# Kernel tuning notes

Hardware: AMD Instinct MI355X
Metric: run time of the kernel (lower is better)

Reference implementation:

```python
import jax, jax.numpy as jnp
import numpy as np

VOCAB, EMB = 100000, 300
B, T = 64, 128
RNN, OUT = 256, 256

def _structure(seed=0):
    # Deterministic forest: sentence b has length T - b (128..65, sorted descending
    # as required by pack_padded_sequence). Each sentence is a random recursive
    # dependency tree: parent[i] ~ U[0, i). node_level = longest path from a leaf,
    # which equals the dgl.prop_nodes_topo frontier index of the node.
    rng = np.random.default_rng(seed)
    lengths = np.array([T - b for b in range(B)], dtype=np.int64)
    offsets = np.concatenate([[0], np.cumsum(lengths)])
    N = int(offsets[-1])
    level = np.zeros(N, np.int64)
    child, parent, tok = [], [], []
    for b in range(B):
        Lb, base = int(lengths[b]), int(offsets[b])
        par = np.zeros(Lb, np.int64)
        for i in range(1, Lb):
            par[i] = rng.integers(0, i)
        lev = np.zeros(Lb, np.int64)
        for i in range(Lb - 1, 0, -1):  # parent index < child index
            lev[par[i]] = max(lev[par[i]], lev[i] + 1)
        level[base:base + Lb] = lev
        child.append(base + np.arange(1, Lb))
        parent.append(base + par[1:])
        tok.append(b * T + np.arange(Lb))
    return (lengths, np.concatenate(child), np.concatenate(parent),
            np.concatenate(tok), level, int(level.max()) + 1)

def setup_inputs() -> dict:
    key = jax.random.key(0)
    ks = jax.random.split(key, 16)
    lengths, child_idx, parent_idx, tok_idx, node_level, n_levels = _structure()
    s = 0.05
    G4, G3, H2 = 4 * RNN, 3 * OUT, 2 * RNN
    return dict(
        embed_ids=jax.random.randint(ks[0], (B, T), 0, VOCAB),
        lengths=jnp.asarray(lengths),
        child_idx=jnp.asarray(child_idx),
        parent_idx=jnp.asarray(parent_idx),
        tok_idx=jnp.asarray(tok_idx),
        node_level=jnp.asarray(node_level),
        n_levels=n_levels,
        emb_table=jax.random.normal(ks[1], (VOCAB, EMB), jnp.float32) * s,
        w_ih_f=jax.random.normal(ks[2], (G4, EMB), jnp.float32) * s,
        w_hh_f=jax.random.normal(ks[3], (G4, RNN), jnp.float32) * s,
        b_f=jax.random.normal(ks[4], (G4,), jnp.float32) * s,
        w_ih_b=jax.random.normal(ks[5], (G4, EMB), jnp.float32) * s,
        w_hh_b=jax.random.normal(ks[6], (G4, RNN), jnp.float32) * s,
        b_b=jax.random.normal(ks[7], (G4,), jnp.float32) * s,
        W_iou=jax.random.normal(ks[8], (G3, H2), jnp.float32) * s,
        U_iou=jax.random.normal(ks[9], (G3, OUT), jnp.float32) * s,
        b_iou=jax.random.normal(ks[10], (G3,), jnp.float32) * s,
        U_f=jax.random.normal(ks[11], (OUT, OUT), jnp.float32) * s,
        b_uf=jax.random.normal(ks[12], (OUT,), jnp.float32) * s,
        W_hid=jax.random.normal(ks[13], (OUT, H2), jnp.float32) * s,
        b_hid=jax.random.normal(ks[14], (OUT,), jnp.float32) * s,
    )

def _lstm(x, Wih, Whh, b):
    # x: [B, T, E] -> hidden states [B, T, H]; PyTorch gate order i, f, g, o
    Bn, H = x.shape[0], Whh.shape[1]
    def step(carry, xt):
        h, c = carry
        g = xt @ Wih.T + h @ Whh.T + b
        i, f, gg, o = jnp.split(g, 4, axis=-1)
        c = jax.nn.sigmoid(f) * c + jax.nn.sigmoid(i) * jnp.tanh(gg)
        h = jax.nn.sigmoid(o) * jnp.tanh(c)
        return (h, c), h
    h0 = jnp.zeros((Bn, H), x.dtype)
    _, hs = jax.lax.scan(step, (h0, h0), jnp.swapaxes(x, 0, 1))
    return jnp.swapaxes(hs, 0, 1)

def _forward(embed_ids, lengths, child_idx, parent_idx, tok_idx, node_level, n_levels,
             emb_table, w_ih_f, w_hh_f, b_f, w_ih_b, w_hh_b, b_b,
             W_iou, U_iou, b_iou, U_f, b_uf, W_hid, b_hid):
    x = emb_table[embed_ids]                                  # [B,T,E]; dropout = identity (eval)
    h_f = _lstm(x, w_ih_f, w_hh_f, b_f)
    # Backward direction over TRUE lengths only (pack_padded semantics):
    # per-row involution t -> len-1-t for t < len, identity on padding.
    t = jnp.arange(T)
    ridx = jnp.where(t[None, :] < lengths[:, None], lengths[:, None] - 1 - t[None, :], t[None, :])
    x_rev = jnp.take_along_axis(x, ridx[:, :, None], axis=1)
    h_b = jnp.take_along_axis(_lstm(x_rev, w_ih_b, w_hh_b, b_b), ridx[:, :, None], axis=1)
    h_seq = jnp.concatenate([h_f, h_b], axis=-1).reshape(B * T, 2 * RNN)
    hx = h_seq[tok_idx]                                       # [N, 2*RNN] valid tokens, flattened
    N = hx.shape[0]
    iou_acc = hx @ W_iou.T                                    # g.ndata['iou'] (W_iou has no bias)
    h = hx @ W_hid.T + b_hid                                  # initial g.ndata['h'] (overwritten by apply)
    c = jnp.zeros((N, OUT), hx.dtype)                         # g.ndata['c']
    c_red = jnp.zeros((N, OUT), hx.dtype)                     # reduced child cell states
    clev = node_level[child_idx]
    for l in range(n_levels):                                 # topological frontiers, leaves -> roots
        m = (node_level == l)[:, None]
        i_, o_, u_ = jnp.split(iou_acc + b_iou, 3, axis=-1)   # apply_node_func
        c_new = jax.nn.sigmoid(i_) * jnp.tanh(u_) + c_red
        h_new = jax.nn.sigmoid(o_) * jnp.tanh(c_new)
        h = jnp.where(m, h_new, h)
        c = jnp.where(m, c_new, c)
        # message + reduce: children at level l send to parents; U_iou is linear so
        # per-child accumulation equals U_iou(sum of child h) at the parent.
        em = (clev == l).astype(hx.dtype)[:, None]
        hc, cc = h[child_idx], c[child_idx]
        iou_acc = iou_acc + jax.ops.segment_sum(em * (hc @ U_iou.T), parent_idx, num_segments=N)
        f = jax.nn.sigmoid(hc @ U_f.T + b_uf)
        c_red = c_red + jax.ops.segment_sum(em * (f * cc), parent_idx, num_segments=N)
    return h                                                  # g.ndata.pop('h'): [N, OUT]

def reference(embed_ids, lengths, child_idx, parent_idx, tok_idx, node_level, n_levels,
              emb_table, w_ih_f, w_hh_f, b_f, w_ih_b, w_hh_b, b_b,
              W_iou, U_iou, b_iou, U_f, b_uf, W_hid, b_hid):
    return _forward(embed_ids, lengths, child_idx, parent_idx, tok_idx, node_level, n_levels,
                    emb_table, w_ih_f, w_hh_f, b_f, w_ih_b, w_hh_b, b_b,
                    W_iou, U_iou, b_iou, U_f, b_uf, W_hid, b_hid)
```

## Files before the change

### kernel.cpp

```cpp
#include <hip/hip_runtime.h>
#include <hip/hip_fp16.h>
#include <cstdint>
#include <cstddef>

#define TT 128
#define HID 256
#define GG4 1024
#define GG3 768

typedef _Float16 f16x2 __attribute__((ext_vector_type(2)));
typedef _Float16 f16x8 __attribute__((ext_vector_type(8)));
typedef short    bf16x8 __attribute__((ext_vector_type(8)));
typedef float    f32x4 __attribute__((ext_vector_type(4)));

union f16x8u { f16x8 v; f16x2 p[4]; uint4 q; };

__device__ __forceinline__ float sigf(float x){ return 1.f/(1.f+__expf(-x)); }
__device__ __forceinline__ float tanh_(float x){
  float cx = fminf(fmaxf(x,-15.f),15.f);
  float e = __expf(2.f*cx);
  return (e-1.f)/(e+1.f);
}

__device__ __forceinline__ float dot2(f16x2 a, f16x2 b, float c){
#if __has_builtin(__builtin_amdgcn_fdot2)
  return __builtin_amdgcn_fdot2(a, b, c, false);
#else
  return c + (float)a[0]*(float)b[0] + (float)a[1]*(float)b[1];
#endif
}

__device__ __forceinline__ ushort f2bf(float x){
  union { float f; uint32_t u; } v; v.f = x;
  uint32_t r = v.u + 0x7FFF + ((v.u >> 16) & 1);
  return (ushort)(r >> 16);
}

__global__ __launch_bounds__(256) void prep_kernel(
    const int* __restrict__ ids, const float* __restrict__ emb, ushort* __restrict__ xh,
    const float* __restrict__ wihf, ushort* __restrict__ wtihf,
    const float* __restrict__ wihb, ushort* __restrict__ wtihb,
    const float* __restrict__ Wiou, ushort* __restrict__ wiouh,
    const float* __restrict__ whhf, const float* __restrict__ whhb,
    _Float16* __restrict__ wtf, _Float16* __restrict__ wtb,
    const float* __restrict__ Uiou, const float* __restrict__ Uf,
    ushort* __restrict__ UTbf)
{
  for (int it = blockIdx.x*256 + threadIdx.x; it < 557056; it += gridDim.x*256) {
    if (it < 327680) {
      int m = it / 40, q = it - m*40;
      int k0 = q << 3;
      int id = ids[m];
      ushort o[8];
#pragma unroll
      for (int j = 0; j < 8; j++) {
        int k = k0 + j;
        o[j] = (k < 300) ? f2bf(emb[(size_t)id*300 + k]) : (ushort)0;
      }
      *(uint4*)&xh[(size_t)m*320 + k0] = *(uint4*)o;
    } else if (it < 409600) {
      int i2 = it - 327680;
      const float* src = wihf; ushort* dst = wtihf;
      if (i2 >= 40960) { i2 -= 40960; src = wihb; dst = wtihb; }
      int r = i2 / 40, q = i2 - r*40;
      int k0 = q << 3;
      ushort o[8];
#pragma unroll
      for (int j = 0; j < 8; j++) {
        int k = k0 + j;
        o[j] = (k < 300) ? f2bf(src[(size_t)r*300 + k]) : (ushort)0;
      }
      *(uint4*)&dst[(size_t)r*320 + k0] = *(uint4*)o;
    } else if (it < 458752) {
      int i2 = it - 409600;
      int r = i2 >> 6, k0 = (i2 & 63) << 3;
      ushort o[8];
#pragma unroll
      for (int j = 0; j < 8; j++) o[j] = f2bf(Wiou[(size_t)r*512 + k0 + j]);
      *(uint4*)&wiouh[(size_t)r*512 + k0] = *(uint4*)o;
    } else if (it < 524288) {
      int i2 = it - 458752;
      int dir = i2 >> 15, rem = i2 & 32767;
      int k8 = rem >> 10, g = rem & 1023;
      const float* w = dir ? whhb : whhf;
      _Float16*   wt = dir ? wtb  : wtf;
      f16x8 pk;
#pragma unroll
      for (int j = 0; j < 8; j++) pk[j] = (_Float16)w[(size_t)g*HID + (k8<<3) + j];
      *(f16x8*)&wt[(((size_t)k8<<10) + g) << 3] = pk;
    } else {
      int i2 = it - 524288;
      int r = i2 >> 5, c = (i2 & 31) << 3;
      const float* src = (r < GG3) ? &Uiou[(size_t)r*HID + c] : &Uf[(size_t)(r-GG3)*HID + c];
      ushort o[8];
#pragma unroll
      for (int j = 0; j < 8; j++) o[j] = f2bf(src[j]);
      *(uint4*)&UTbf[(size_t)r*HID + c] = *(uint4*)o;
    }
  }
}

template<bool BIAS>
__global__ __launch_bounds__(256) void mfma_gemm_kernel(
    const ushort* __restrict__ A, const ushort* __restrict__ Bt,
    const float* __restrict__ bias, float* __restrict__ C,
    int M, int N, int ksteps)
{
  constexpr int LDS_ROW = 40;
  __shared__ ushort As[128*LDS_ROW];
  __shared__ ushort Bs[128*LDS_ROW];
  const int tid = threadIdx.x;
  const int m0 = blockIdx.x * 128, n0 = blockIdx.y * 128;
  const int wave = tid >> 6, lane = tid & 63;
  const int wm = (wave >> 1) * 64, wn = (wave & 1) * 64;
  const int fr = lane & 15;
  const int fk = (lane >> 4) << 3;
  const size_t Kp = (size_t)ksteps << 5;
  const int r0_ = tid >> 2,        k0_ = (tid & 3) << 3;
  const int r1_ = (tid + 256) >> 2, k1_ = ((tid + 256) & 3) << 3;
  f32x4 acc[4][4] = {};
  {
    uint4 av0 = make_uint4(0,0,0,0), av1 = make_uint4(0,0,0,0);
    if (m0 + r0_ < M) av0 = *(const uint4*)&A[(size_t)(m0+r0_)*Kp + k0_];
    if (m0 + r1_ < M) av1 = *(const uint4*)&A[(size_t)(m0+r1_)*Kp + k1_];
    const uint4 bv0 = *(const uint4*)&Bt[(size_t)(n0+r0_)*Kp + k0_];
    const uint4 bv1 = *(const uint4*)&Bt[(size_t)(n0+r1_)*Kp + k1_];
    *(uint4*)&As[r0_*LDS_ROW + k0_] = av0;
    *(uint4*)&As[r1_*LDS_ROW + k1_] = av1;
    *(uint4*)&Bs[r0_*LDS_ROW + k0_] = bv0;
    *(uint4*)&Bs[r1_*LDS_ROW + k1_] = bv1;
  }
  __syncthreads();
  for (int ks = 0; ks < ksteps; ks++) {
    uint4 nav0 = make_uint4(0,0,0,0), nav1 = make_uint4(0,0,0,0);
    uint4 nbv0 = make_uint4(0,0,0,0), nbv1 = make_uint4(0,0,0,0);
    const bool more = (ks + 1 < ksteps);
    if (more) {
      const int kb = (ks + 1) << 5;
      if (m0 + r0_ < M) nav0 = *(const uint4*)&A[(size_t)(m0+r0_)*Kp + kb + k0_];
      if (m0 + r1_ < M) nav1 = *(const uint4*)&A[(size_t)(m0+r1_)*Kp + kb + k1_];
      nbv0 = *(const uint4*)&Bt[(size_t)(n0+r0_)*Kp + kb + k0_];
      nbv1 = *(const uint4*)&Bt[(size_t)(n0+r1_)*Kp + kb + k1_];
    }
    bf16x8 af[4], bfr[4];
#pragma unroll
    for (int i = 0; i < 4; i++) {
      af[i]  = *(const bf16x8*)&As[(wm + i*16 + fr)*LDS_ROW + fk];
      bfr[i] = *(const bf16x8*)&Bs[(wn + i*16 + fr)*LDS_ROW + fk];
    }
#pragma unroll
    for (int mi = 0; mi < 4; mi++)
#pragma unroll
      for (int ni = 0; ni < 4; ni++)
        acc[mi][ni] = __builtin_amdgcn_mfma_f32_16x16x32_bf16(af[mi], bfr[ni], acc[mi][ni], 0, 0, 0);
    __syncthreads();
    if (more) {
      *(uint4*)&As[r0_*LDS_ROW + k0_] = nav0;
      *(uint4*)&As[r1_*LDS_ROW + k1_] = nav1;
      *(uint4*)&Bs[r0_*LDS_ROW + k0_] = nbv0;
      *(uint4*)&Bs[r1_*LDS_ROW + k1_] = nbv1;
      __syncthreads();
    }
  }
  const int drow = (lane >> 4) << 2, dcol = lane & 15;
#pragma unroll
  for (int mi = 0; mi < 4; mi++) {
#pragma unroll
    for (int ni = 0; ni < 4; ni++) {
      const int col = n0 + wn + ni*16 + dcol;
      const float bv = BIAS ? bias[col] : 0.f;
#pragma unroll
      for (int r = 0; r < 4; r++) {
        const int row = m0 + wm + mi*16 + drow + r;
        if (row < M) C[(size_t)row*N + col] = acc[mi][ni][r] + bv;
      }
    }
  }
}

#define RCH 23
__global__ __launch_bounds__(512, 2) void lstm_kernel(
    const float* __restrict__ xgf, const float* __restrict__ xgb,
    const _Float16* __restrict__ wtf, const _Float16* __restrict__ wtb,
    const int* __restrict__ lengths,
    float* __restrict__ hsf, float* __restrict__ hsb)
{
  const int b8  = blockIdx.x & 7;
  const int dir = b8 >> 2;
  const int p   = (blockIdx.x >> 3) * 4 + (b8 & 3);
  const int r0 = 2*p, r1 = r0 + 1;
  const float* __restrict__ xg = dir ? xgb : xgf;
  const _Float16* __restrict__ wt = dir ? wtb : wtf;
  float* __restrict__ hs = dir ? hsb : hsf;
  const int t = threadIdx.x;
  const int u = t & 255;

  extern __shared__ char smem[];
  f16x8*    wl  = (f16x8*)smem;
  _Float16* hb  = (_Float16*)(smem + 147456);
  float*    exf = (float*)(smem + 147456 + 1024);
  float*    exo = exf + 512;

  uint4 wr0[RCH], wr1[RCH];
#pragma unroll
  for (int c = 0; c < RCH; c++) {
    wr0[c] = *(const uint4*)&wt[(((size_t)c << 10) + t) << 3];
    wr1[c] = *(const uint4*)&wt[(((size_t)c << 10) + t + 512) << 3];
  }
#pragma unroll
  for (int c = 0; c < RCH; c++) {
    asm volatile("" : "+v"(wr0[c].x), "+v"(wr0[c].y), "+v"(wr0[c].z), "+v"(wr0[c].w));
    asm volatile("" : "+v"(wr1[c].x), "+v"(wr1[c].y), "+v"(wr1[c].z), "+v"(wr1[c].w));
  }
#pragma unroll
  for (int c = RCH; c < 32; c++) {
    wl[((c - RCH)*2 + 0)*512 + t] = *(const f16x8*)&wt[(((size_t)c << 10) + t) << 3];
    wl[((c - RCH)*2 + 1)*512 + t] = *(const f16x8*)&wt[(((size_t)c << 10) + t + 512) << 3];
  }
  if (t < 256) { hb[t] = (_Float16)0.f; hb[256 + t] = (_Float16)0.f; }
  __syncthreads();

  const int len0 = lengths[r0], len1 = lengths[r1];
  float c0 = 0.f, c1 = 0.f;
  for (int s = 0; s < len0; s++) {
    const bool a1 = s < len1;
    const int t0 = dir ? (len0 - 1 - s) : s;
    const int t1 = dir ? (len1 - 1 - s) : s;
    const float* xr0 = xg + ((size_t)r0*TT + t0)*GG4;
    const float xa0 = xr0[t], xb0 = xr0[t + 512];
    float xa1 = 0.f, xb1 = 0.f;
    if (a1) {
      const float* xr1 = xg + ((size_t)r1*TT + t1)*GG4;
      xa1 = xr1[t]; xb1 = xr1[t + 512];
    }
    float aa0 = 0.f, aa1 = 0.f, ab0 = 0.f, ab1 = 0.f;
#pragma unroll
    for (int k8 = 0; k8 < 32; k8++) {
      f16x8u w0, w1, h0, h1;
      if (k8 < RCH) { w0.q = wr0[k8]; w1.q = wr1[k8]; }
      else {
        w0.v = wl[((k8 - RCH)*2 + 0)*512 + t];
        w1.v = wl[((k8 - RCH)*2 + 1)*512 + t];
      }
      h0.v = *(const f16x8*)&hb[k8 << 3];
      h1.v = *(const f16x8*)&hb[256 + (k8 << 3)];
#pragma unroll
      for (int j = 0; j < 4; j++) {
        aa0 = dot2(w0.p[j], h0.p[j], aa0);
        aa1 = dot2(w0.p[j], h1.p[j], aa1);
        ab0 = dot2(w1.p[j], h0.p[j], ab0);
        ab1 = dot2(w1.p[j], h1.p[j], ab1);
      }
    }
    if (t >= 256) {
      exf[u]       = aa0 + xa0;  exf[256 + u] = aa1 + xa1;
      exo[u]       = ab0 + xb0;  exo[256 + u] = ab1 + xb1;
    }
    __syncthreads();
    if (t < 256) {
      {
        const float ig = sigf(aa0 + xa0);
        const float gg = tanh_(ab0 + xb0);
        const float fg = sigf(exf[u]);
        const float og = sigf(exo[u]);
        c0 = fg*c0 + ig*gg;
        const float h = og*tanh_(c0);
        hb[u] = (_Float16)h;
        hs[((size_t)r0*TT + t0)*HID + u] = h;
      }
      if (a1) {
        const float ig = sigf(aa1 + xa1);
        const float gg = tanh_(ab1 + xb1);
        const float fg = sigf(exf[256 + u]);
        const float og = sigf(exo[256 + u]);
        c1 = fg*c1 + ig*gg;
        const float h = og*tanh_(c1);
        hb[256 + u] = (_Float16)h;
        hs[((size_t)r1*TT + t1)*HID + u] = h;
      }
    }
    __syncthreads();
  }
}

__global__ __launch_bounds__(256) void gather_hx_kernel(
    const int* __restrict__ tok, const float* __restrict__ hsf,
    const float* __restrict__ hsb, ushort* __restrict__ hxh, int Nn)
{
  int it = blockIdx.x*256 + threadIdx.x;
  if (it >= Nn*64) return;
  int n = it >> 6, q = it & 63;
  int k0 = q << 3;
  int tk = tok[n];
  int b = tk >> 7, t = tk & 127;
  const float* src = (k0 < 256) ? &hsf[((size_t)b*TT + t)*HID + k0]
                                : &hsb[((size_t)b*TT + t)*HID + (k0 - 256)];
  ushort o[8];
#pragma unroll
  for (int j = 0; j < 8; j++) o[j] = f2bf(src[j]);
  *(uint4*)&hxh[(size_t)n*512 + k0] = *(uint4*)o;
}

__global__ __launch_bounds__(1024) void csr_kernel(
    const int* __restrict__ child_idx, const int* __restrict__ parent_idx,
    int* __restrict__ choff, int* __restrict__ chlist,
    int* __restrict__ deg , int E, int Nn)
{
  __shared__ int part[1024];
  const int tid = threadIdx.x;
  for (int e = tid; e < E; e += 1024) atomicAdd(&deg[parent_idx[e]], 1);
  __syncthreads();
  int loc[8]; int s = 0;
#pragma unroll
  for (int m = 0; m < 8; m++) {
    const int i = tid*8 + m;
    loc[m] = s;
    s += (i < Nn) ? deg[i] : 0;
  }
  part[tid] = s;
  __syncthreads();
  for (int off = 1; off < 1024; off <<= 1) {
    int v = (tid >= off) ? part[tid - off] : 0;
    __syncthreads();
    part[tid] += v;
    __syncthreads();
  }
  const int pre = (tid > 0) ? part[tid-1] : 0;
#pragma unroll
  for (int m = 0; m < 8; m++) {
    const int i = tid*8 + m;
    if (i < Nn) choff[i] = pre + loc[m];
  }
  if (tid == 1023) choff[Nn] = part[1023];
  __syncthreads();
#pragma unroll
  for (int m = 0; m < 8; m++) {
    const int i = tid*8 + m;
    if (i < Nn) deg[i] = pre + loc[m];
  }
  __syncthreads();
  for (int e = tid; e < E; e += 1024) {
    int pos = atomicAdd(&deg[parent_idx[e]], 1);
    chlist[pos] = child_idx[e];
  }
}

__global__ __launch_bounds__(128) void tree_sort_kernel(
    const int* __restrict__ lengths, const int* __restrict__ node_level,
    int* __restrict__ tnlist, int* __restrict__ tlvloff, int* __restrict__ tnlv)
{
  const int b = blockIdx.x, tid = threadIdx.x;
  __shared__ int hist[130], cur[129];
  __shared__ int off_s, len_s, mx;
  if (tid == 0) {
    int o = 0;
    for (int i = 0; i < b; i++) o += lengths[i];
    off_s = o; len_s = lengths[b]; mx = 1;
  }
  for (int i = tid; i < 130; i += 128) hist[i] = 0;
  __syncthreads();
  const int off = off_s, len = len_s;
  for (int i = tid; i < len; i += 128) {
    int lv = node_level[off + i];
    atomicAdd(&hist[lv], 1);
    atomicMax(&mx, lv + 1);
  }
  __syncthreads();
  if (tid == 0) {
    int s = 0;
    for (int l = 0; l < 129; l++) { cur[l] = s; tlvloff[b*130 + l] = s; s += hist[l]; }
    tlvloff[b*130 + 129] = s;
    tnlv[b] = mx;
  }
  __syncthreads();
  for (int i = tid; i < len; i += 128) {
    int lv = node_level[off + i];
    int pos = atomicAdd(&cur[lv], 1);
    tnlist[b*128 + pos] = off + i;
  }
}

__global__ __launch_bounds__(512) void tree_kernel(
    const int* __restrict__ tnlist, const int* __restrict__ tlvloff,
    const int* __restrict__ tnlv,
    const int* __restrict__ choff, const int* __restrict__ chlist,
    const ushort* __restrict__ UTbf,
    const float* __restrict__ biou, const float* __restrict__ buf_,
    const float* __restrict__ iou,
    float* __restrict__ um, float* __restrict__ fm,
    float* __restrict__ hout)
{
  const int b = blockIdx.x;
  const int tid = threadIdx.x;
  const int nlv = tnlv[b];
  const int* __restrict__ nl = tnlist + b*128;
  const int* __restrict__ lo = tlvloff + b*130;
  __shared__ ushort hl[16][264];
  __shared__ float  cl[16][260];
  __shared__ int    nid[16];
  const int j5 = tid >> 5, lane5 = tid & 31;
  const int wave = tid >> 6, lane = tid & 63;
  const int fr16 = lane & 15, khalf = lane >> 4;
  for (int l = 0; l < nlv; l++) {
    const int na = lo[l], ne = lo[l+1];
    for (int g0 = na; g0 < ne; g0 += 16) {
      __syncthreads();
      const int n = (g0 + j5 < ne) ? nl[g0 + j5] : -1;
      if (lane5 == 0) nid[j5] = n;
      if (n >= 0) {
        f32x4 a[8];
#pragma unroll
        for (int q = 0; q < 8; q++) {
          const int d = (q*32 + lane5) << 2;
          if (d < GG3) a[q] = *(const f32x4*)&iou[(size_t)n*GG3 + d];
          else         a[q] = (f32x4){0.f, 0.f, 0.f, 0.f};
        }
        const int e0 = choff[n], e1 = choff[n+1];
        for (int eb = e0; eb < e1; eb += 4) {
          int ch4[4];
#pragma unroll
          for (int i = 0; i < 4; i++) ch4[i] = (eb + i < e1) ? chlist[eb + i] : -1;
#pragma unroll
          for (int i = 0; i < 4; i++) {
            const int ch = ch4[i];
            if (ch >= 0) {
#pragma unroll
              for (int q = 0; q < 8; q++) {
                const int d = (q*32 + lane5) << 2;
                const f32x4 v = (d < GG3)
                  ? *(const f32x4*)&um[(size_t)ch*GG3 + d]
                  : *(const f32x4*)&fm[(size_t)ch*HID + (d - GG3)];
                a[q] += v;
              }
            }
          }
        }
#pragma unroll
        for (int qq = 0; qq < 2; qq++) {
#pragma unroll
          for (int i = 0; i < 4; i++) {
            const int u = qq*128 + (lane5 << 2) + i;
            const float i_ = a[qq][i]   + biou[u];
            const float o_ = a[qq+2][i] + biou[256 + u];
            const float uu = a[qq+4][i] + biou[512 + u];
            const float cv = sigf(i_)*tanh_(uu) + a[qq+6][i];
            const float hv = sigf(o_)*tanh_(cv);
            cl[j5][u] = cv;
            hl[j5][u] = f2bf(hv);
            hout[(size_t)n*HID + u] = hv;
          }
        }
      } else {
#pragma unroll
        for (int q = 0; q < 8; q++) hl[j5][(q << 5) + lane5] = 0;
      }
      __syncthreads();
      if (l == nlv - 1) continue;
      bf16x8 af[8];
#pragma unroll
      for (int ks = 0; ks < 8; ks++)
        af[ks] = *(const bf16x8*)&hl[fr16][ks*32 + (khalf << 3)];
      for (int nt = wave; nt < 64; nt += 8) {
        f32x4 dacc = {0.f, 0.f, 0.f, 0.f};
#pragma unroll
        for (int ks = 0; ks < 8; ks++) {
          const bf16x8 bfr = *(const bf16x8*)&UTbf[(size_t)(nt*16 + fr16)*HID + ks*32 + (khalf << 3)];
          dacc = __builtin_amdgcn_mfma_f32_16x16x32_bf16(af[ks], bfr, dacc, 0, 0, 0);
        }
        const int r = nt*16 + fr16;
        if (r < GG3) {
#pragma unroll
          for (int g = 0; g < 4; g++) {
            const int n2 = nid[(khalf << 2) + g];
            if (n2 >= 0) um[(size_t)n2*GG3 + r] = dacc[g];
          }
        } else {
          const int fr = r - GG3;
          const float bv = buf_[fr];
#pragma unroll
          for (int g = 0; g < 4; g++) {
            const int jj = (khalf << 2) + g;
            const int n2 = nid[jj];
            if (n2 >= 0) fm[(size_t)n2*HID + fr] = sigf(dacc[g] + bv) * cl[jj][fr];
          }
        }
      }
    }
  }
}

extern "C" void kernel_launch(void* const* d_in, const int* in_sizes, int n_in,
                              void* d_out, int out_size, void* d_ws, size_t ws_size,
                              hipStream_t stream)
{
  const int*   embed_ids = (const int*)d_in[0];
  const int*   lengths   = (const int*)d_in[1];
  const int*   child_idx = (const int*)d_in[2];
  const int*   parent_idx= (const int*)d_in[3];
  const int*   tok_idx   = (const int*)d_in[4];
  const int*   node_level= (const int*)d_in[5];
  const float* emb  = (const float*)d_in[7];
  const float* wihf = (const float*)d_in[8];
  const float* whhf = (const float*)d_in[9];
  const float* bf   = (const float*)d_in[10];
  const float* wihb = (const float*)d_in[11];
  const float* whhb = (const float*)d_in[12];
  const float* bb   = (const float*)d_in[13];
  const float* Wiou = (const float*)d_in[14];
  const float* Uiou = (const float*)d_in[15];
  const float* biou = (const float*)d_in[16];
  const float* Uf   = (const float*)d_in[17];
  const float* buf_ = (const float*)d_in[18];
  const int E  = in_sizes[2];
  const int Nn = in_sizes[4];
  float* hout = (float*)d_out;

  char* w = (char*)d_ws;
  size_t off = 0;
  auto take = [&](size_t bytes) -> char* {
    char* p = w + off;
    off += (bytes + 255) & ~(size_t)255;
    return p;
  };
  int*      deg   = (int*)     take((size_t)(Nn+1)*4);
  size_t zero_end = off;
  ushort*   xh    = (ushort*)  take((size_t)8192*320*2);
  ushort*   wtihf = (ushort*)  take((size_t)1024*320*2);
  ushort*   wtihb = (ushort*)  take((size_t)1024*320*2);
  ushort*   wiouh = (ushort*)  take((size_t)768*512*2);
  float*    xgf   = (float*)   take((size_t)8192*1024*4);
  float*    xgb   = (float*)   take((size_t)8192*1024*4);
  _Float16* wtf   = (_Float16*)take((size_t)32*1024*8*2);
  _Float16* wtb   = (_Float16*)take((size_t)32*1024*8*2);
  float*    hsf   = (float*)   take((size_t)64*128*256*4);
  float*    hsb   = (float*)   take((size_t)64*128*256*4);
  ushort*   hxh   = (ushort*)  take((size_t)Nn*512*2);
  float*    iou   = (float*)   take((size_t)Nn*GG3*4);
  float*    um    = (float*)   take((size_t)Nn*GG3*4);
  float*    fm    = (float*)   take((size_t)Nn*HID*4);
  ushort*   UTbf  = (ushort*)  take((size_t)1024*256*2);
  int*      tnlist= (int*)     take((size_t)64*128*4);
  int*      tlvloff=(int*)     take((size_t)64*130*4);
  int*      tnlv  = (int*)     take((size_t)64*4);
  int*      choff = (int*)     take((size_t)(Nn+1)*4);
  int*      chlist= (int*)     take((size_t)(E>0?E:1)*4);
  (void)ws_size; (void)n_in; (void)out_size;

  hipMemsetAsync(d_ws, 0, zero_end, stream);
  prep_kernel<<<1024, 256, 0, stream>>>(embed_ids, emb, xh, wihf, wtihf, wihb, wtihb,
                                        Wiou, wiouh, whhf, whhb, wtf, wtb, Uiou, Uf, UTbf);
  mfma_gemm_kernel<true><<<dim3(64, 8), 256, 0, stream>>>(xh, wtihf, bf, xgf, 8192, 1024, 10);
  mfma_gemm_kernel<true><<<dim3(64, 8), 256, 0, stream>>>(xh, wtihb, bb, xgb, 8192, 1024, 10);
  lstm_kernel<<<64, 512, 152576, stream>>>(xgf, xgb, wtf, wtb, lengths, hsf, hsb);
  gather_hx_kernel<<<(Nn*64 + 255)/256, 256, 0, stream>>>(tok_idx, hsf, hsb, hxh, Nn);
  mfma_gemm_kernel<false><<<dim3((Nn + 127)/128, 6), 256, 0, stream>>>(hxh, wiouh, nullptr, iou, Nn, GG3, 16);
  csr_kernel<<<1, 1024, 0, stream>>>(child_idx, parent_idx, choff, chlist, deg, E, Nn);
  tree_sort_kernel<<<64, 128, 0, stream>>>(lengths, node_level, tnlist, tlvloff, tnlv);
  tree_kernel<<<64, 512, 0, stream>>>(tnlist, tlvloff, tnlv, choff, chlist, UTbf,
                                      biou, buf_, iou, um, fm, hout);
}
```

Measured before the change: 908.1 us.

## Merge input GEMMs and graph-prep kernels, batch tree-level U GEMM per level

The forward and backward input-projection GEMMs become one launch using a doubled grid, and the CSR build and per-tree level sort become one 65-block kernel. The tree kernel now evaluates every node of a level before running the U_iou/U_f MFMA pass, loading the U weight fragments into registers once per level instead of once per 16-node group. Cell states move from shared memory to a global buffer so that all of a level's h rows can sit in dynamic shared memory. The asm register pins on the LSTM weights are removed, so the compiler may spill or reload them, and the cell state now takes an extra global round trip.

```diff
diff --git a/kernel.cpp b/kernel.cpp
--- a/kernel.cpp
+++ b/kernel.cpp
@@ -100,11 +100,89 @@
   }
 }
 
-template<bool BIAS>
+__global__ __launch_bounds__(256) void mfma_gemm2_kernel(
+    const ushort* __restrict__ A,
+    const ushort* __restrict__ Btf, const ushort* __restrict__ Btb,
+    const float* __restrict__ bf_, const float* __restrict__ bb_,
+    float* __restrict__ Cf, float* __restrict__ Cb, int M, int N, int ksteps)
+{
+  constexpr int LDS_ROW = 40;
+  __shared__ ushort As[128*LDS_ROW];
+  __shared__ ushort Bs[128*LDS_ROW];
+  const int tid = threadIdx.x;
+  const int dirb = blockIdx.y >> 3;
+  const ushort* __restrict__ Bt = dirb ? Btb : Btf;
+  const float* __restrict__ bias = dirb ? bb_ : bf_;
+  float* __restrict__ C = dirb ? Cb : Cf;
+  const int m0 = blockIdx.x * 128, n0 = (blockIdx.y & 7) * 128;
+  const int wave = tid >> 6, lane = tid & 63;
+  const int wm = (wave >> 1) * 64, wn = (wave & 1) * 64;
+  const int fr = lane & 15;
+  const int fk = (lane >> 4) << 3;
+  const size_t Kp = (size_t)ksteps << 5;
+  const int r0_ = tid >> 2,        k0_ = (tid & 3) << 3;
+  const int r1_ = (tid + 256) >> 2, k1_ = ((tid + 256) & 3) << 3;
+  f32x4 acc[4][4] = {};
+  {
+    const uint4 av0 = *(const uint4*)&A[(size_t)(m0+r0_)*Kp + k0_];
+    const uint4 av1 = *(const uint4*)&A[(size_t)(m0+r1_)*Kp + k1_];
+    const uint4 bv0 = *(const uint4*)&Bt[(size_t)(n0+r0_)*Kp + k0_];
+    const uint4 bv1 = *(const uint4*)&Bt[(size_t)(n0+r1_)*Kp + k1_];
+    *(uint4*)&As[r0_*LDS_ROW + k0_] = av0;
+    *(uint4*)&As[r1_*LDS_ROW + k1_] = av1;
+    *(uint4*)&Bs[r0_*LDS_ROW + k0_] = bv0;
+    *(uint4*)&Bs[r1_*LDS_ROW + k1_] = bv1;
+  }
+  __syncthreads();
+  for (int ks = 0; ks < ksteps; ks++) {
+    uint4 nav0, nav1, nbv0, nbv1;
+    const bool more = (ks + 1 < ksteps);
+    if (more) {
+      const int kb = (ks + 1) << 5;
+      nav0 = *(const uint4*)&A[(size_t)(m0+r0_)*Kp + kb + k0_];
+      nav1 = *(const uint4*)&A[(size_t)(m0+r1_)*Kp + kb + k1_];
+      nbv0 = *(const uint4*)&Bt[(size_t)(n0+r0_)*Kp + kb + k0_];
+      nbv1 = *(const uint4*)&Bt[(size_t)(n0+r1_)*Kp + kb + k1_];
+    }
+    bf16x8 af[4], bfr[4];
+#pragma unroll
+    for (int i = 0; i < 4; i++) {
+      af[i]  = *(const bf16x8*)&As[(wm + i*16 + fr)*LDS_ROW + fk];
+      bfr[i] = *(const bf16x8*)&Bs[(wn + i*16 + fr)*LDS_ROW + fk];
+    }
+#pragma unroll
+    for (int mi = 0; mi < 4; mi++)
+#pragma unroll
+      for (int ni = 0; ni < 4; ni++)
+        acc[mi][ni] = __builtin_amdgcn_mfma_f32_16x16x32_bf16(af[mi], bfr[ni], acc[mi][ni], 0, 0, 0);
+    __syncthreads();
+    if (more) {
+      *(uint4*)&As[r0_*LDS_ROW + k0_] = nav0;
+      *(uint4*)&As[r1_*LDS_ROW + k1_] = nav1;
+      *(uint4*)&Bs[r0_*LDS_ROW + k0_] = nbv0;
+      *(uint4*)&Bs[r1_*LDS_ROW + k1_] = nbv1;
+      __syncthreads();
+    }
+  }
+  const int drow = (lane >> 4) << 2, dcol = lane & 15;
+#pragma unroll
+  for (int mi = 0; mi < 4; mi++) {
+#pragma unroll
+    for (int ni = 0; ni < 4; ni++) {
+      const int col = n0 + wn + ni*16 + dcol;
+      const float bv = bias[col];
+#pragma unroll
+      for (int r = 0; r < 4; r++) {
+        const int row = m0 + wm + mi*16 + drow + r;
+        C[(size_t)row*N + col] = acc[mi][ni][r] + bv;
+      }
+    }
+  }
+}
+
 __global__ __launch_bounds__(256) void mfma_gemm_kernel(
     const ushort* __restrict__ A, const ushort* __restrict__ Bt,
-    const float* __restrict__ bias, float* __restrict__ C,
-    int M, int N, int ksteps)
+    float* __restrict__ C, int M, int N, int ksteps)
 {
   constexpr int LDS_ROW = 40;
   __shared__ ushort As[128*LDS_ROW];
@@ -168,11 +246,10 @@
 #pragma unroll
     for (int ni = 0; ni < 4; ni++) {
       const int col = n0 + wn + ni*16 + dcol;
-      const float bv = BIAS ? bias[col] : 0.f;
 #pragma unroll
       for (int r = 0; r < 4; r++) {
         const int row = m0 + wm + mi*16 + drow + r;
-        if (row < M) C[(size_t)row*N + col] = acc[mi][ni][r] + bv;
+        if (row < M) C[(size_t)row*N + col] = acc[mi][ni][r];
       }
     }
   }
@@ -206,11 +283,6 @@
   for (int c = 0; c < RCH; c++) {
     wr0[c] = *(const uint4*)&wt[(((size_t)c << 10) + t) << 3];
     wr1[c] = *(const uint4*)&wt[(((size_t)c << 10) + t + 512) << 3];
-  }
-#pragma unroll
-  for (int c = 0; c < RCH; c++) {
-    asm volatile("" : "+v"(wr0[c].x), "+v"(wr0[c].y), "+v"(wr0[c].z), "+v"(wr0[c].w));
-    asm volatile("" : "+v"(wr1[c].x), "+v"(wr1[c].y), "+v"(wr1[c].z), "+v"(wr1[c].w));
   }
 #pragma unroll
   for (int c = RCH; c < 32; c++) {
@@ -301,82 +373,81 @@
   *(uint4*)&hxh[(size_t)n*512 + k0] = *(uint4*)o;
 }
 
-__global__ __launch_bounds__(1024) void csr_kernel(
+__global__ __launch_bounds__(1024) void graph_kernel(
+    const int* __restrict__ lengths, const int* __restrict__ node_level,
     const int* __restrict__ child_idx, const int* __restrict__ parent_idx,
+    int* __restrict__ tnlist, int* __restrict__ tlvloff, int* __restrict__ tnlv,
     int* __restrict__ choff, int* __restrict__ chlist,
     int* __restrict__ deg , int E, int Nn)
 {
-  __shared__ int part[1024];
   const int tid = threadIdx.x;
-  for (int e = tid; e < E; e += 1024) atomicAdd(&deg[parent_idx[e]], 1);
-  __syncthreads();
-  int loc[8]; int s = 0;
-#pragma unroll
-  for (int m = 0; m < 8; m++) {
-    const int i = tid*8 + m;
-    loc[m] = s;
-    s += (i < Nn) ? deg[i] : 0;
-  }
-  part[tid] = s;
-  __syncthreads();
-  for (int off = 1; off < 1024; off <<= 1) {
-    int v = (tid >= off) ? part[tid - off] : 0;
-    __syncthreads();
-    part[tid] += v;
-    __syncthreads();
-  }
-  const int pre = (tid > 0) ? part[tid-1] : 0;
-#pragma unroll
-  for (int m = 0; m < 8; m++) {
-    const int i = tid*8 + m;
-    if (i < Nn) choff[i] = pre + loc[m];
-  }
-  if (tid == 1023) choff[Nn] = part[1023];
-  __syncthreads();
-#pragma unroll
-  for (int m = 0; m < 8; m++) {
-    const int i = tid*8 + m;
-    if (i < Nn) deg[i] = pre + loc[m];
-  }
-  __syncthreads();
-  for (int e = tid; e < E; e += 1024) {
-    int pos = atomicAdd(&deg[parent_idx[e]], 1);
-    chlist[pos] = child_idx[e];
-  }
-}
-
-__global__ __launch_bounds__(128) void tree_sort_kernel(
-    const int* __restrict__ lengths, const int* __restrict__ node_level,
-    int* __restrict__ tnlist, int* __restrict__ tlvloff, int* __restrict__ tnlv)
-{
-  const int b = blockIdx.x, tid = threadIdx.x;
-  __shared__ int hist[130], cur[129];
-  __shared__ int off_s, len_s, mx;
-  if (tid == 0) {
-    int o = 0;
-    for (int i = 0; i < b; i++) o += lengths[i];
-    off_s = o; len_s = lengths[b]; mx = 1;
-  }
-  for (int i = tid; i < 130; i += 128) hist[i] = 0;
-  __syncthreads();
-  const int off = off_s, len = len_s;
-  for (int i = tid; i < len; i += 128) {
-    int lv = node_level[off + i];
-    atomicAdd(&hist[lv], 1);
-    atomicMax(&mx, lv + 1);
-  }
-  __syncthreads();
-  if (tid == 0) {
-    int s = 0;
-    for (int l = 0; l < 129; l++) { cur[l] = s; tlvloff[b*130 + l] = s; s += hist[l]; }
-    tlvloff[b*130 + 129] = s;
-    tnlv[b] = mx;
-  }
-  __syncthreads();
-  for (int i = tid; i < len; i += 128) {
-    int lv = node_level[off + i];
-    int pos = atomicAdd(&cur[lv], 1);
-    tnlist[b*128 + pos] = off + i;
+  if (blockIdx.x < 64) {
+    const int b = blockIdx.x;
+    __shared__ int hist[130], cur[129];
+    __shared__ int off_s, len_s, mx;
+    if (tid == 0) {
+      int o = 0;
+      for (int i = 0; i < b; i++) o += lengths[i];
+      off_s = o; len_s = lengths[b]; mx = 1;
+    }
+    for (int i = tid; i < 130; i += 1024) hist[i] = 0;
+    __syncthreads();
+    const int off = off_s, len = len_s;
+    for (int i = tid; i < len; i += 1024) {
+      int lv = node_level[off + i];
+      atomicAdd(&hist[lv], 1);
+      atomicMax(&mx, lv + 1);
+    }
+    __syncthreads();
+    if (tid == 0) {
+      int s = 0;
+      for (int l = 0; l < 129; l++) { cur[l] = s; tlvloff[b*130 + l] = s; s += hist[l]; }
+      tlvloff[b*130 + 129] = s;
+      tnlv[b] = mx;
+    }
+    __syncthreads();
+    for (int i = tid; i < len; i += 1024) {
+      int lv = node_level[off + i];
+      int pos = atomicAdd(&cur[lv], 1);
+      tnlist[b*128 + pos] = off + i;
+    }
+  } else {
+    __shared__ int part[1024];
+    for (int e = tid; e < E; e += 1024) atomicAdd(&deg[parent_idx[e]], 1);
+    __syncthreads();
+    int loc[8]; int s = 0;
+#pragma unroll
+    for (int m = 0; m < 8; m++) {
+      const int i = tid*8 + m;
+      loc[m] = s;
+      s += (i < Nn) ? deg[i] : 0;
+    }
+    part[tid] = s;
+    __syncthreads();
+    for (int off = 1; off < 1024; off <<= 1) {
+      int v = (tid >= off) ? part[tid - off] : 0;
+      __syncthreads();
+      part[tid] += v;
+      __syncthreads();
+    }
+    const int pre = (tid > 0) ? part[tid-1] : 0;
+#pragma unroll
+    for (int m = 0; m < 8; m++) {
+      const int i = tid*8 + m;
+      if (i < Nn) choff[i] = pre + loc[m];
+    }
+    if (tid == 1023) choff[Nn] = part[1023];
+    __syncthreads();
+#pragma unroll
+    for (int m = 0; m < 8; m++) {
+      const int i = tid*8 + m;
+      if (i < Nn) deg[i] = pre + loc[m];
+    }
+    __syncthreads();
+    for (int e = tid; e < E; e += 1024) {
+      int pos = atomicAdd(&deg[parent_idx[e]], 1);
+      chlist[pos] = child_idx[e];
+    }
   }
 }
 
@@ -388,25 +459,27 @@
     const float* __restrict__ biou, const float* __restrict__ buf_,
     const float* __restrict__ iou,
     float* __restrict__ um, float* __restrict__ fm,
-    float* __restrict__ hout)
+    float* __restrict__ cbuf, float* __restrict__ hout)
 {
   const int b = blockIdx.x;
   const int tid = threadIdx.x;
   const int nlv = tnlv[b];
   const int* __restrict__ nl = tnlist + b*128;
   const int* __restrict__ lo = tlvloff + b*130;
-  __shared__ ushort hl[16][264];
-  __shared__ float  cl[16][260];
-  __shared__ int    nid[16];
+  extern __shared__ char tsm[];
+  ushort* hl  = (ushort*)tsm;
+  int*    nid = (int*)(tsm + 128*264*2);
   const int j5 = tid >> 5, lane5 = tid & 31;
   const int wave = tid >> 6, lane = tid & 63;
   const int fr16 = lane & 15, khalf = lane >> 4;
   for (int l = 0; l < nlv; l++) {
     const int na = lo[l], ne = lo[l+1];
-    for (int g0 = na; g0 < ne; g0 += 16) {
-      __syncthreads();
-      const int n = (g0 + j5 < ne) ? nl[g0 + j5] : -1;
-      if (lane5 == 0) nid[j5] = n;
+    const int nL = ne - na;
+    const int mT = (nL + 15) >> 4;
+    for (int g0 = 0; g0 < (mT << 4); g0 += 16) {
+      const int jn = g0 + j5;
+      const int n = (jn < nL) ? nl[na + jn] : -1;
+      if (lane5 == 0) nid[jn] = n;
       if (n >= 0) {
         f32x4 a[8];
 #pragma unroll
@@ -445,47 +518,50 @@
             const float uu = a[qq+4][i] + biou[512 + u];
             const float cv = sigf(i_)*tanh_(uu) + a[qq+6][i];
             const float hv = sigf(o_)*tanh_(cv);
-            cl[j5][u] = cv;
-            hl[j5][u] = f2bf(hv);
+            cbuf[(size_t)n*HID + u] = cv;
+            hl[jn*264 + u] = f2bf(hv);
             hout[(size_t)n*HID + u] = hv;
           }
         }
       } else {
 #pragma unroll
-        for (int q = 0; q < 8; q++) hl[j5][(q << 5) + lane5] = 0;
-      }
-      __syncthreads();
-      if (l == nlv - 1) continue;
-      bf16x8 af[8];
-#pragma unroll
-      for (int ks = 0; ks < 8; ks++)
-        af[ks] = *(const bf16x8*)&hl[fr16][ks*32 + (khalf << 3)];
+        for (int q = 0; q < 8; q++) hl[jn*264 + (q << 5) + lane5] = 0;
+      }
+    }
+    __syncthreads();
+    if (l < nlv - 1) {
       for (int nt = wave; nt < 64; nt += 8) {
-        f32x4 dacc = {0.f, 0.f, 0.f, 0.f};
-#pragma unroll
-        for (int ks = 0; ks < 8; ks++) {
-          const bf16x8 bfr = *(const bf16x8*)&UTbf[(size_t)(nt*16 + fr16)*HID + ks*32 + (khalf << 3)];
-          dacc = __builtin_amdgcn_mfma_f32_16x16x32_bf16(af[ks], bfr, dacc, 0, 0, 0);
-        }
+        bf16x8 bfr[8];
         const int r = nt*16 + fr16;
-        if (r < GG3) {
-#pragma unroll
-          for (int g = 0; g < 4; g++) {
-            const int n2 = nid[(khalf << 2) + g];
-            if (n2 >= 0) um[(size_t)n2*GG3 + r] = dacc[g];
+#pragma unroll
+        for (int ks = 0; ks < 8; ks++)
+          bfr[ks] = *(const bf16x8*)&UTbf[(size_t)r*HID + ks*32 + (khalf << 3)];
+        for (int mt = 0; mt < mT; mt++) {
+          f32x4 dacc = {0.f, 0.f, 0.f, 0.f};
+#pragma unroll
+          for (int ks = 0; ks < 8; ks++) {
+            const bf16x8 af = *(const bf16x8*)&hl[(mt*16 + fr16)*264 + ks*32 + (khalf << 3)];
+            dacc = __builtin_amdgcn_mfma_f32_16x16x32_bf16(af, bfr[ks], dacc, 0, 0, 0);
           }
-        } else {
-          const int fr = r - GG3;
-          const float bv = buf_[fr];
-#pragma unroll
-          for (int g = 0; g < 4; g++) {
-            const int jj = (khalf << 2) + g;
-            const int n2 = nid[jj];
-            if (n2 >= 0) fm[(size_t)n2*HID + fr] = sigf(dacc[g] + bv) * cl[jj][fr];
+          if (r < GG3) {
+#pragma unroll
+            for (int g = 0; g < 4; g++) {
+              const int n2 = nid[mt*16 + (khalf << 2) + g];
+              if (n2 >= 0) um[(size_t)n2*GG3 + r] = dacc[g];
+            }
+          } else {
+            const int fr = r - GG3;
+            const float bv = buf_[fr];
+#pragma unroll
+            for (int g = 0; g < 4; g++) {
+              const int n2 = nid[mt*16 + (khalf << 2) + g];
+              if (n2 >= 0) fm[(size_t)n2*HID + fr] = sigf(dacc[g] + bv) * cbuf[(size_t)n2*HID + fr];
+            }
           }
         }
       }
     }
+    __syncthreads();
   }
 }
 
@@ -538,6 +614,7 @@
   float*    iou   = (float*)   take((size_t)Nn*GG3*4);
   float*    um    = (float*)   take((size_t)Nn*GG3*4);
   float*    fm    = (float*)   take((size_t)Nn*HID*4);
+  float*    cbuf  = (float*)   take((size_t)Nn*HID*4);
   ushort*   UTbf  = (ushort*)  take((size_t)1024*256*2);
   int*      tnlist= (int*)     take((size_t)64*128*4);
   int*      tlvloff=(int*)     take((size_t)64*130*4);
@@ -549,13 +626,12 @@
   hipMemsetAsync(d_ws, 0, zero_end, stream);
   prep_kernel<<<1024, 256, 0, stream>>>(embed_ids, emb, xh, wihf, wtihf, wihb, wtihb,
                                         Wiou, wiouh, whhf, whhb, wtf, wtb, Uiou, Uf, UTbf);
-  mfma_gemm_kernel<true><<<dim3(64, 8), 256, 0, stream>>>(xh, wtihf, bf, xgf, 8192, 1024, 10);
-  mfma_gemm_kernel<true><<<dim3(64, 8), 256, 0, stream>>>(xh, wtihb, bb, xgb, 8192, 1024, 10);
+  mfma_gemm2_kernel<<<dim3(64, 16), 256, 0, stream>>>(xh, wtihf, wtihb, bf, bb, xgf, xgb, 8192, 1024, 10);
   lstm_kernel<<<64, 512, 152576, stream>>>(xgf, xgb, wtf, wtb, lengths, hsf, hsb);
   gather_hx_kernel<<<(Nn*64 + 255)/256, 256, 0, stream>>>(tok_idx, hsf, hsb, hxh, Nn);
-  mfma_gemm_kernel<false><<<dim3((Nn + 127)/128, 6), 256, 0, stream>>>(hxh, wiouh, nullptr, iou, Nn, GG3, 16);
-  csr_kernel<<<1, 1024, 0, stream>>>(child_idx, parent_idx, choff, chlist, deg, E, Nn);
-  tree_sort_kernel<<<64, 128, 0, stream>>>(lengths, node_level, tnlist, tlvloff, tnlv);
-  tree_kernel<<<64, 512, 0, stream>>>(tnlist, tlvloff, tnlv, choff, chlist, UTbf,
-                                      biou, buf_, iou, um, fm, hout);
-}
+  mfma_gemm_kernel<<<dim3((Nn + 127)/128, 6), 256, 0, stream>>>(hxh, wiouh, iou, Nn, GG3, 16);
+  graph_kernel<<<65, 1024, 0, stream>>>(lengths, node_level, child_idx, parent_idx,
+                                        tnlist, tlvloff, tnlv, choff, chlist, deg, E, Nn);
+  tree_kernel<<<64, 512, 68096, stream>>>(tnlist, tlvloff, tnlv, choff, chlist, UTbf,
+                                          biou, buf_, iou, um, fm, cbuf, hout);
+}
```

New measurement: 781.5 us. 1.16x faster.
